# Performance work log

Hardware: AMD Instinct MI355X
Metric: run time of the kernel (lower is better)

The kernel has to match this reference:

```python
import jax, jax.numpy as jnp
import numpy as np

EMB = 1024
N_HEADS = 16
HEAD_SIZE = 64
BLOCK_SIZE = 1024
YARN_ALPHA = 1.0
TRAINING = False  # eval mode: NTK_alpha = seq_len / block_size, dropout = identity


def yarn_rope(x, seq_len):
    # x: [B, H, S, D]
    i = jnp.arange(0, HEAD_SIZE, 2, dtype=x.dtype)
    ntk_alpha = 1.0 if TRAINING else seq_len / BLOCK_SIZE
    inv_freq = 1.0 / (10000.0 ** (i / (HEAD_SIZE * ntk_alpha)))
    pos = jnp.arange(seq_len, dtype=x.dtype)
    yarn_scaling = (1.0 / jnp.sqrt(1.0 + YARN_ALPHA * (pos / BLOCK_SIZE) ** 2))[:, None]  # [S,1]
    theta = pos[:, None] * inv_freq[None, :] * yarn_scaling  # [S, D/2]
    sin = jnp.sin(theta)[None, None, :, :]
    cos = jnp.cos(theta)[None, None, :, :]
    x_even = x[..., 0::2]
    x_odd = x[..., 1::2]
    ev = x_even * cos - x_odd * sin
    od = x_even * sin + x_odd * cos
    # interleave back: [..., D/2, 2] -> [..., D]
    return jnp.stack([ev, od], axis=-1).reshape(x.shape)


def setup_inputs() -> dict:
    key = jax.random.key(0)
    ks = jax.random.split(key, 6)
    B, S = 4, 2048
    scale = 1.0 / np.sqrt(EMB)
    return {
        "x": jax.random.normal(ks[0], (B, S, EMB), dtype=jnp.float32),
        "Wq": jax.random.normal(ks[1], (EMB, EMB), dtype=jnp.float32) * scale,
        "Wk": jax.random.normal(ks[2], (EMB, EMB), dtype=jnp.float32) * scale,
        "Wv": jax.random.normal(ks[3], (EMB, EMB), dtype=jnp.float32) * scale,
        "Wp": jax.random.normal(ks[4], (EMB, EMB), dtype=jnp.float32) * scale,
        "bp": jnp.zeros((EMB,), dtype=jnp.float32),
    }


def reference(x, Wq, Wk, Wv, Wp, bp):
    B, S, E = x.shape
    def heads(w):
        # nn.Linear: y = x @ W.T ; then view(B,S,H,D).permute(0,2,1,3)
        return (x @ w.T).reshape(B, S, N_HEADS, HEAD_SIZE).transpose(0, 2, 1, 3)
    q = yarn_rope(heads(Wq), S)
    k = yarn_rope(heads(Wk), S)
    v = heads(Wv)
    score = jnp.einsum('bhqd,bhkd->bhqk', q, k) * (HEAD_SIZE ** -0.5)
    causal = jnp.tril(jnp.ones((S, S), dtype=bool))
    score = jnp.where(causal[None, None], score, -jnp.inf)
    score = jax.nn.softmax(score, axis=-1)
    out = jnp.einsum('bhqk,bhkd->bhqd', score, v)
    # faithful to source: contiguous().view(B, S, E) directly on (B,H,S,D)
    out = out.reshape(B, S, E)
    out = out @ Wp.T + bp  # dropout is identity in eval
    return out
```

## Files before the change

### kernel.cpp

```cpp
#include <hip/hip_runtime.h>
#include <stdint.h>

#define EMB 1024
#define NHEADS 16
#define HDIM 64
#define BB 4
#define SS 2048
#define MR (BB*SS)

typedef float f32x4 __attribute__((ext_vector_type(4)));
typedef short s16x8 __attribute__((ext_vector_type(8)));
typedef unsigned short u16;
typedef u16 u16x8 __attribute__((ext_vector_type(8)));

__device__ __forceinline__ float bf2f(u16 h){
  union{uint32_t u;float f;} v; v.u = ((uint32_t)h)<<16; return v.f;
}
__device__ __forceinline__ u16 f2bf(float f){
  union{float f;uint32_t u;} v; v.f=f; uint32_t u=v.u;
  return (u16)((u + 0x7FFFu + ((u>>16)&1u)) >> 16);
}

__device__ __forceinline__ void stage16(const void* g, void* lds_base){
  __builtin_amdgcn_global_load_lds(
      (__attribute__((address_space(1))) void*)(g),
      (__attribute__((address_space(3))) void*)(lds_base),
      16, 0, 0);
}

__global__ void k_tables(float2* __restrict__ tab){
  int idx = blockIdx.x*256 + threadIdx.x;
  if (idx >= SS*32) return;
  int s = idx >> 5, j = idx & 31;
  double ntk = (double)SS / 1024.0;
  double invf = pow(10000.0, -((double)(2*j))/(64.0*ntk));
  double p = (double)s / 1024.0;
  double scal = 1.0 / sqrt(1.0 + p*p);
  double th = (double)s * invf * scal;
  tab[idx] = make_float2((float)cos(th), (float)sin(th));
}

__global__ void k_cvt(const float* __restrict__ in, u16* __restrict__ out, int n){
  int i = (blockIdx.x*256 + threadIdx.x)*4;
  if (i >= n) return;
  float4 v = *(const float4*)(in + i);
  union{u16 a[4]; uint64_t q;} pk;
  pk.a[0]=f2bf(v.x); pk.a[1]=f2bf(v.y); pk.a[2]=f2bf(v.z); pk.a[3]=f2bf(v.w);
  *(uint64_t*)(out + i) = pk.q;
}

template<int MODE>
__global__ __launch_bounds__(256) void k_gemm(
    const u16* __restrict__ A, const u16* __restrict__ B,
    u16* __restrict__ Cq, u16* __restrict__ Ck, u16* __restrict__ VT,
    const float* __restrict__ bias, float* __restrict__ Cf,
    const float2* __restrict__ tab)
{
  constexpr int K = EMB;
  __shared__ u16 As[128][32];
  __shared__ u16 Bs[128][32];
  const int tid = threadIdx.x, lane = tid & 63, wave = tid >> 6;
  const int wr = wave >> 1, wc = wave & 1;
  const int m0 = blockIdx.x*128, n0 = blockIdx.y*128;

  f32x4 acc[4][4];
  #pragma unroll
  for (int i=0;i<4;i++)
    #pragma unroll
    for (int j=0;j<4;j++)
      #pragma unroll
      for (int r=0;r<4;r++) acc[i][j][r] = 0.f;

  const int cl = lane & 15, kq = (lane>>4)*8, rg = lane>>4;
  char* AsB = (char*)&As[0][0];
  char* BsB = (char*)&Bs[0][0];
  const int wbase = wave*1024;

  for (int k0 = 0; k0 < K; k0 += 32) {
    __syncthreads();
    #pragma unroll
    for (int p=0;p<2;p++){
      int c = p*256 + tid;
      int row = c>>2, sub = c&3;
      stage16(A + (size_t)(m0+row)*K + k0 + sub*8, AsB + p*4096 + wbase);
      stage16(B + (size_t)(n0+row)*K + k0 + sub*8, BsB + p*4096 + wbase);
    }
    __syncthreads();
    s16x8 a[4], b[4];
    #pragma unroll
    for (int i=0;i<4;i++){
      a[i] = *(const s16x8*)&As[wr*64 + i*16 + cl][kq];
      b[i] = *(const s16x8*)&Bs[wc*64 + i*16 + cl][kq];
    }
    #pragma unroll
    for (int i=0;i<4;i++)
      #pragma unroll
      for (int j=0;j<4;j++)
        acc[i][j] = __builtin_amdgcn_mfma_f32_16x16x32_bf16(a[i], b[j], acc[i][j], 0, 0, 0);
  }

  if constexpr (MODE==1){
    #pragma unroll
    for (int i=0;i<4;i++)
      #pragma unroll
      for (int j=0;j<4;j++){
        int col = n0 + wc*64 + j*16 + cl;
        #pragma unroll
        for (int r=0;r<4;r++){
          int row = m0 + wr*64 + i*16 + rg*4 + r;
          Cf[(size_t)row*EMB + col] = acc[i][j][r] + bias[col];
        }
      }
  } else {
    const int colbase = n0 + wc*64;
    #pragma unroll
    for (int i=0;i<4;i++)
      #pragma unroll
      for (int j=0;j<4;j++){
        int col = colbase + j*16 + cl;
        if (col < 2048) {
          u16* dst = (col < 1024) ? Cq : Ck;
          int cc = col & 1023;
          int dp = (col & 63) >> 1;
          #pragma unroll
          for (int r=0;r<4;r++){
            int row = m0 + wr*64 + i*16 + rg*4 + r;
            int s = row & (SS-1);
            float own = acc[i][j][r];
            float par = __shfl_xor(own, 1, 64);
            float2 cs = tab[s*32 + dp];
            float outv = (cl & 1) ? (par*cs.y + own*cs.x)
                                  : (own*cs.x - par*cs.y);
            dst[(size_t)row*EMB + cc] = f2bf(outv);
          }
        } else {
          int dfull = col - 2048;
          int h = dfull >> 6, d = dfull & 63;
          int row0 = m0 + wr*64 + i*16 + rg*4;
          int bb = row0 >> 11, s0 = row0 & (SS-1);
          union{u16 a4[4]; uint64_t q;} pk;
          #pragma unroll
          for (int r=0;r<4;r++) pk.a4[r] = f2bf(acc[i][j][r]);
          *(uint64_t*)(VT + ((size_t)(bb*NHEADS + h)*64 + d)*SS + s0) = pk.q;
        }
      }
  }
}

__global__ __launch_bounds__(256) void k_attn(
    const u16* __restrict__ qg, const u16* __restrict__ kg,
    const u16* __restrict__ vt, u16* __restrict__ o)
{
  __shared__ u16 Qs[128*64];
  __shared__ u16 Ks[2][64*64];
  __shared__ u16 Vs[2][64*64];

  const int tid = threadIdx.x, lane = tid&63, wave = tid>>6;
  const int cl = lane&15, rg = lane>>4;
  const int rg4 = rg*4;
  const int bh = blockIdx.x;
  const int q0 = (SS/128 - 1 - blockIdx.y)*128;
  const int b = bh>>4, h = bh&15;
  const size_t qk0 = (size_t)b*SS*EMB + h*64;
  const u16* vtb = vt + (size_t)bh*64*SS;
  const int wbase = wave*1024;

  const int rowbase = q0 + wave*32;
  const int nt = (q0 + 128)/64;

  #pragma unroll
  for (int p=0;p<4;p++){
    int c = p*256+tid, row = c>>3, j = c&7;
    int d0 = ((j ^ (row&7))<<3);
    stage16(qg + qk0 + (size_t)(q0+row)*EMB + d0, (char*)Qs + p*4096 + wbase);
  }
  #pragma unroll
  for (int p=0;p<2;p++){
    int c = p*256+tid, row = c>>3, j = c&7;
    int d0 = ((j ^ (row&7))<<3);
    stage16(kg + qk0 + (size_t)row*EMB + d0, (char*)Ks[0] + p*4096 + wbase);
    stage16(vtb + (size_t)row*SS + d0,       (char*)Vs[0] + p*4096 + wbase);
  }
  __syncthreads();

  s16x8 qf[2][2];
  #pragma unroll
  for (int mi=0;mi<2;mi++)
    #pragma unroll
    for (int kk2=0;kk2<2;kk2++){
      int row = wave*32 + mi*16 + cl;
      qf[mi][kk2] = *(const s16x8*)&Qs[row*64 + (((kk2*4+rg) ^ (row&7))<<3)];
    }

  u16* PsW = Qs + wave*2048;

  float mrun[2], lrun[2];
  f32x4 oacc[2][4];
  #pragma unroll
  for (int i=0;i<2;i++){ mrun[i] = -1e30f; lrun[i] = 0.f; }
  #pragma unroll
  for (int i=0;i<2;i++)
    #pragma unroll
    for (int j=0;j<4;j++)
      #pragma unroll
      for (int r=0;r<4;r++) oacc[i][j][r] = 0.f;

  const float SCL = 0.125f * 1.44269504088896340736f;

  for (int t=0;t<nt;t++){
    const int kv0 = t*64;
    const int cur = t&1;

    if (t+1 < nt){
      int kv1 = kv0 + 64;
      #pragma unroll
      for (int p=0;p<2;p++){
        int c = p*256+tid, row = c>>3, j = c&7;
        int d0 = ((j ^ (row&7))<<3);
        stage16(kg + qk0 + (size_t)(kv1+row)*EMB + d0, (char*)Ks[cur^1] + p*4096 + wbase);
        stage16(vtb + (size_t)row*SS + kv1 + d0,       (char*)Vs[cur^1] + p*4096 + wbase);
      }
    }

    if (kv0 <= rowbase + 31) {
      f32x4 st[4][2];
      #pragma unroll
      for (int i=0;i<4;i++)
        #pragma unroll
        for (int j=0;j<2;j++)
          #pragma unroll
          for (int r=0;r<4;r++) st[i][j][r] = 0.f;

      #pragma unroll
      for (int kk2=0;kk2<2;kk2++){
        s16x8 kf[4];
        #pragma unroll
        for (int nk=0;nk<4;nk++){
          int row = nk*16+cl;
          kf[nk] = *(const s16x8*)&Ks[cur][row*64 + (((kk2*4+rg) ^ (row&7))<<3)];
        }
        #pragma unroll
        for (int nk=0;nk<4;nk++)
          #pragma unroll
          for (int mq=0;mq<2;mq++)
            st[nk][mq] = __builtin_amdgcn_mfma_f32_16x16x32_bf16(kf[nk], qf[mq][kk2], st[nk][mq], 0,0,0);
      }

      const bool full = (kv0 + 63) <= rowbase;
      float mx[2];
      if (full) {
        #pragma unroll
        for (int mq=0;mq<2;mq++){
          float a0 = -1e30f, a1 = -1e30f;
          #pragma unroll
          for (int nk=0;nk<4;nk++){
            #pragma unroll
            for (int r=0;r<4;r++){
              float vv = st[nk][mq][r]*SCL;
              st[nk][mq][r] = vv;
              if (r&1) a1 = fmaxf(a1, vv); else a0 = fmaxf(a0, vv);
            }
          }
          float m0 = fmaxf(a0, a1);
          m0 = fmaxf(m0, __shfl_xor(m0, 16, 64));
          m0 = fmaxf(m0, __shfl_xor(m0, 32, 64));
          mx[mq] = m0;
        }
      } else {
        #pragma unroll
        for (int mq=0;mq<2;mq++){
          int qgr = rowbase + mq*16 + cl;
          float a0 = -1e30f, a1 = -1e30f;
          #pragma unroll
          for (int nk=0;nk<4;nk++){
            #pragma unroll
            for (int r=0;r<4;r++){
              float vv = st[nk][mq][r]*SCL;
              int kgi = kv0 + nk*16 + rg4 + r;
              vv = (kgi<=qgr) ? vv : -1e30f;
              st[nk][mq][r] = vv;
              if (r&1) a1 = fmaxf(a1, vv); else a0 = fmaxf(a0, vv);
            }
          }
          float m0 = fmaxf(a0, a1);
          m0 = fmaxf(m0, __shfl_xor(m0, 16, 64));
          m0 = fmaxf(m0, __shfl_xor(m0, 32, 64));
          mx[mq] = m0;
        }
      }

      bool need = (mx[0] > mrun[0] + 8.f) || (mx[1] > mrun[1] + 8.f);
      if (__any(need)) {
        #pragma unroll
        for (int mq=0;mq<2;mq++){
          float mn = fmaxf(mrun[mq], mx[mq]);
          float corr = __builtin_amdgcn_exp2f(mrun[mq] - mn);
          mrun[mq] = mn;
          lrun[mq] *= corr;
          #pragma unroll
          for (int r=0;r<4;r++){
            float cb = __shfl(corr, (lane & 48) | (rg4 + r), 64);
            #pragma unroll
            for (int nj=0;nj<4;nj++) oacc[mq][nj][r] *= cb;
          }
        }
      }

      #pragma unroll
      for (int mq=0;mq<2;mq++){
        float rs = 0.f;
        #pragma unroll
        for (int nk=0;nk<4;nk++){
          #pragma unroll
          for (int r=0;r<4;r++){
            float pv = __builtin_amdgcn_exp2f(st[nk][mq][r] - mrun[mq]);
            st[nk][mq][r] = pv; rs += pv;
          }
        }
        lrun[mq] += rs;

        int q = mq*16 + cl;
        #pragma unroll
        for (int nk=0;nk<4;nk++){
          uint32_t pk01, pk23;
          asm("v_cvt_pk_bf16_f32 %0, %1, %2" : "=v"(pk01) : "v"(st[nk][mq][0]), "v"(st[nk][mq][1]));
          asm("v_cvt_pk_bf16_f32 %0, %1, %2" : "=v"(pk23) : "v"(st[nk][mq][2]), "v"(st[nk][mq][3]));
          int k0e = nk*16 + rg4;
          int ch = k0e>>3, el = k0e&7;
          char* p = (char*)PsW + q*128 + ((ch ^ (q&7))<<4) + el*2;
          *(uint2*)p = make_uint2(pk01, pk23);
        }
      }

      #pragma unroll
      for (int kk2=0;kk2<2;kk2++){
        s16x8 pf[2], vf[4];
        #pragma unroll
        for (int mi=0;mi<2;mi++){
          int row = mi*16+cl;
          pf[mi] = *(const s16x8*)&PsW[row*64 + (((kk2*4+rg) ^ (row&7))<<3)];
        }
        #pragma unroll
        for (int nj=0;nj<4;nj++){
          int row = nj*16+cl;
          vf[nj] = *(const s16x8*)&Vs[cur][row*64 + (((kk2*4+rg) ^ (row&7))<<3)];
        }
        #pragma unroll
        for (int mi=0;mi<2;mi++)
          #pragma unroll
          for (int nj=0;nj<4;nj++)
            oacc[mi][nj] = __builtin_amdgcn_mfma_f32_16x16x32_bf16(pf[mi], vf[nj], oacc[mi][nj], 0,0,0);
      }
    }

    __syncthreads();
  }

  #pragma unroll
  for (int mi=0;mi<2;mi++){
    float lsum = lrun[mi];
    lsum += __shfl_xor(lsum, 16, 64);
    lsum += __shfl_xor(lsum, 32, 64);
    #pragma unroll
    for (int r=0;r<4;r++){
      float lb = __shfl(lsum, (lane & 48) | (rg4 + r), 64);
      float linv = 1.f / lb;
      int row = rowbase + mi*16 + rg4 + r;
      int sp = h*128 + (row>>4);
      int epb = (row&15)*64;
      #pragma unroll
      for (int nj=0;nj<4;nj++)
        o[((size_t)b*SS + sp)*EMB + epb + nj*16 + cl] = f2bf(oacc[mi][nj][r]*linv);
    }
  }
}

extern "C" void kernel_launch(void* const* d_in, const int* in_sizes, int n_in,
                              void* d_out, int out_size, void* d_ws, size_t ws_size,
                              hipStream_t stream)
{
  const float* x  = (const float*)d_in[0];
  const float* Wq = (const float*)d_in[1];
  const float* Wk = (const float*)d_in[2];
  const float* Wv = (const float*)d_in[3];
  const float* Wp = (const float*)d_in[4];
  const float* bp = (const float*)d_in[5];
  float* out = (float*)d_out;

  char* ws = (char*)d_ws;
  const size_t XE = (size_t)MR*EMB*2;
  const size_t WE = (size_t)EMB*EMB*2;
  u16* xb  = (u16*)ws; ws += XE;
  u16* wqb = (u16*)ws; ws += WE;
  u16* wkb = (u16*)ws; ws += WE;
  u16* wvb = (u16*)ws; ws += WE;
  u16* wpb = (u16*)ws; ws += WE;
  u16* qb  = (u16*)ws; ws += XE;
  u16* kb  = (u16*)ws; ws += XE;
  u16* vtb = (u16*)ws; ws += XE;
  float2* tab = (float2*)ws; ws += (size_t)SS*32*sizeof(float2);
  u16* ob  = xb;

  k_tables<<<(SS*32+255)/256, 256, 0, stream>>>(tab);
  k_cvt<<<(MR*EMB/4+255)/256, 256, 0, stream>>>(x,  xb,  MR*EMB);
  k_cvt<<<(EMB*EMB/4+255)/256, 256, 0, stream>>>(Wq, wqb, EMB*EMB);
  k_cvt<<<(EMB*EMB/4+255)/256, 256, 0, stream>>>(Wk, wkb, EMB*EMB);
  k_cvt<<<(EMB*EMB/4+255)/256, 256, 0, stream>>>(Wv, wvb, EMB*EMB);
  k_cvt<<<(EMB*EMB/4+255)/256, 256, 0, stream>>>(Wp, wpb, EMB*EMB);

  dim3 g1(MR/128, 3*EMB/128);
  k_gemm<0><<<g1, 256, 0, stream>>>(xb, wqb, qb, kb, vtb, nullptr, nullptr, tab);

  k_attn<<<dim3(BB*NHEADS, SS/128), 256, 0, stream>>>(qb, kb, vtb, ob);

  dim3 g2(MR/128, EMB/128);
  k_gemm<1><<<g2, 256, 0, stream>>>(ob, wpb, nullptr, nullptr, nullptr, bp, out, nullptr);
}
```

Measured before the change: 201.2 us.

## Double-buffer GEMM LDS tiles and fuse prep kernels into one launch

The GEMM now keeps two LDS buffers and issues the global-to-LDS loads for the next K tile before running the MFMAs on the current one, with one barrier per iteration instead of two. This is meant to hide global load latency behind compute. The six setup kernels (the rope table and five bf16 conversions) are merged into one launch to cut launch overhead. LDS use per block doubles, which may lower occupancy. The async LDS loads must also finish before the end-of-loop barrier for the prefetch to be safe.

```diff
diff --git a/kernel.cpp b/kernel.cpp
--- a/kernel.cpp
+++ b/kernel.cpp
@@ -28,25 +28,37 @@
       16, 0, 0);
 }
 
-__global__ void k_tables(float2* __restrict__ tab){
-  int idx = blockIdx.x*256 + threadIdx.x;
-  if (idx >= SS*32) return;
-  int s = idx >> 5, j = idx & 31;
-  double ntk = (double)SS / 1024.0;
-  double invf = pow(10000.0, -((double)(2*j))/(64.0*ntk));
-  double p = (double)s / 1024.0;
-  double scal = 1.0 / sqrt(1.0 + p*p);
-  double th = (double)s * invf * scal;
-  tab[idx] = make_float2((float)cos(th), (float)sin(th));
-}
-
-__global__ void k_cvt(const float* __restrict__ in, u16* __restrict__ out, int n){
-  int i = (blockIdx.x*256 + threadIdx.x)*4;
-  if (i >= n) return;
-  float4 v = *(const float4*)(in + i);
-  union{u16 a[4]; uint64_t q;} pk;
-  pk.a[0]=f2bf(v.x); pk.a[1]=f2bf(v.y); pk.a[2]=f2bf(v.z); pk.a[3]=f2bf(v.w);
-  *(uint64_t*)(out + i) = pk.q;
+__global__ void k_prep(const float* __restrict__ x,
+                       const float* __restrict__ Wq, const float* __restrict__ Wk,
+                       const float* __restrict__ Wv, const float* __restrict__ Wp,
+                       u16* __restrict__ xb, u16* __restrict__ wb,
+                       float2* __restrict__ tab){
+  unsigned g = blockIdx.x*256 + threadIdx.x;
+  if (g < 2097152u){
+    unsigned i = g*4;
+    float4 v = *(const float4*)(x + i);
+    union{u16 a[4]; uint64_t q;} pk;
+    pk.a[0]=f2bf(v.x); pk.a[1]=f2bf(v.y); pk.a[2]=f2bf(v.z); pk.a[3]=f2bf(v.w);
+    *(uint64_t*)(xb + i) = pk.q;
+  } else if (g < 3145728u){
+    unsigned e = (g - 2097152u)*4;
+    unsigned w = e >> 20;
+    unsigned off = e & 1048575u;
+    const float* s = (w==0)?Wq:(w==1)?Wk:(w==2)?Wv:Wp;
+    float4 v = *(const float4*)(s + off);
+    union{u16 a[4]; uint64_t q;} pk;
+    pk.a[0]=f2bf(v.x); pk.a[1]=f2bf(v.y); pk.a[2]=f2bf(v.z); pk.a[3]=f2bf(v.w);
+    *(uint64_t*)(wb + e) = pk.q;
+  } else {
+    unsigned idx = g - 3145728u;
+    int s = idx >> 5, j = idx & 31;
+    double ntk = (double)SS / 1024.0;
+    double invf = pow(10000.0, -((double)(2*j))/(64.0*ntk));
+    double p = (double)s / 1024.0;
+    double scal = 1.0 / sqrt(1.0 + p*p);
+    double th = (double)s * invf * scal;
+    tab[idx] = make_float2((float)cos(th), (float)sin(th));
+  }
 }
 
 template<int MODE>
@@ -57,8 +69,8 @@
     const float2* __restrict__ tab)
 {
   constexpr int K = EMB;
-  __shared__ u16 As[128][32];
-  __shared__ u16 Bs[128][32];
+  __shared__ u16 As[2][128][32];
+  __shared__ u16 Bs[2][128][32];
   const int tid = threadIdx.x, lane = tid & 63, wave = tid >> 6;
   const int wr = wave >> 1, wc = wave & 1;
   const int m0 = blockIdx.x*128, n0 = blockIdx.y*128;
@@ -72,31 +84,41 @@
       for (int r=0;r<4;r++) acc[i][j][r] = 0.f;
 
   const int cl = lane & 15, kq = (lane>>4)*8, rg = lane>>4;
-  char* AsB = (char*)&As[0][0];
-  char* BsB = (char*)&Bs[0][0];
+  char* AsB = (char*)&As[0][0][0];
+  char* BsB = (char*)&Bs[0][0][0];
   const int wbase = wave*1024;
+  const int row_s = (tid>>2), sub8 = (tid&3)*8;
+
+  #pragma unroll
+  for (int p=0;p<2;p++){
+    int c = p*256 + tid, row = c>>2, sub = c&3;
+    stage16(A + (size_t)(m0+row)*K + sub*8, AsB + p*4096 + wbase);
+    stage16(B + (size_t)(n0+row)*K + sub*8, BsB + p*4096 + wbase);
+  }
+  __syncthreads();
 
   for (int k0 = 0; k0 < K; k0 += 32) {
-    __syncthreads();
-    #pragma unroll
-    for (int p=0;p<2;p++){
-      int c = p*256 + tid;
-      int row = c>>2, sub = c&3;
-      stage16(A + (size_t)(m0+row)*K + k0 + sub*8, AsB + p*4096 + wbase);
-      stage16(B + (size_t)(n0+row)*K + k0 + sub*8, BsB + p*4096 + wbase);
-    }
-    __syncthreads();
+    const int cur = (k0>>5)&1;
+    if (k0 + 32 < K){
+      #pragma unroll
+      for (int p=0;p<2;p++){
+        int c = p*256 + tid, row = c>>2, sub = c&3;
+        stage16(A + (size_t)(m0+row)*K + k0+32 + sub*8, AsB + (cur^1)*8192 + p*4096 + wbase);
+        stage16(B + (size_t)(n0+row)*K + k0+32 + sub*8, BsB + (cur^1)*8192 + p*4096 + wbase);
+      }
+    }
     s16x8 a[4], b[4];
     #pragma unroll
     for (int i=0;i<4;i++){
-      a[i] = *(const s16x8*)&As[wr*64 + i*16 + cl][kq];
-      b[i] = *(const s16x8*)&Bs[wc*64 + i*16 + cl][kq];
+      a[i] = *(const s16x8*)&As[cur][wr*64 + i*16 + cl][kq];
+      b[i] = *(const s16x8*)&Bs[cur][wc*64 + i*16 + cl][kq];
     }
     #pragma unroll
     for (int i=0;i<4;i++)
       #pragma unroll
       for (int j=0;j<4;j++)
         acc[i][j] = __builtin_amdgcn_mfma_f32_16x16x32_bf16(a[i], b[j], acc[i][j], 0, 0, 0);
+    __syncthreads();
   }
 
   if constexpr (MODE==1){
@@ -400,13 +422,9 @@
   u16* vtb = (u16*)ws; ws += XE;
   float2* tab = (float2*)ws; ws += (size_t)SS*32*sizeof(float2);
   u16* ob  = xb;
-
-  k_tables<<<(SS*32+255)/256, 256, 0, stream>>>(tab);
-  k_cvt<<<(MR*EMB/4+255)/256, 256, 0, stream>>>(x,  xb,  MR*EMB);
-  k_cvt<<<(EMB*EMB/4+255)/256, 256, 0, stream>>>(Wq, wqb, EMB*EMB);
-  k_cvt<<<(EMB*EMB/4+255)/256, 256, 0, stream>>>(Wk, wkb, EMB*EMB);
-  k_cvt<<<(EMB*EMB/4+255)/256, 256, 0, stream>>>(Wv, wvb, EMB*EMB);
-  k_cvt<<<(EMB*EMB/4+255)/256, 256, 0, stream>>>(Wp, wpb, EMB*EMB);
+  (void)wkb; (void)wvb;
+
+  k_prep<<<12544, 256, 0, stream>>>(x, Wq, Wk, Wv, Wp, xb, wqb, tab);
 
   dim3 g1(MR/128, 3*EMB/128);
   k_gemm<0><<<g1, 256, 0, stream>>>(xb, wqb, qb, kb, vtb, nullptr, nullptr, tab);
```

Result: faster. 185.1 us (-8.0%).
